# Kernel tuning notes

Measured on AMD Instinct MI355X. Metric: run time of the kernel, lower is better.

Reference implementation:

```python
import jax, jax.numpy as jnp
import numpy as np

DIM = 96; QK = 96; MLP = 192; HEADS = 6; NTOK = 8; GS = 128; KS = 5
B, D, H, W = 2, 8, 64, 64


def _ln(x, g, b, eps=1e-5):
    m = x.mean(-1, keepdims=True)
    v = x.var(-1, keepdims=True)
    return (x - m) / jnp.sqrt(v + eps) * g + b


def _l2(x, eps=1e-12):
    n = jnp.linalg.norm(x, axis=-1, keepdims=True)
    return x / jnp.maximum(n, eps)


def setup_inputs() -> dict:
    key = jax.random.key(0)
    ks = jax.random.split(key, 16)
    p = lambda i, shape: jax.random.normal(ks[i], shape, jnp.float32) * 0.02
    return dict(
        x=jax.random.normal(ks[0], (B, DIM, D, H, W), jnp.float32),
        means=jax.random.normal(ks[1], (NTOK, DIM), jnp.float32),
        ln1_g=jnp.ones((DIM,), jnp.float32), ln1_b=jnp.zeros((DIM,), jnp.float32),
        Wkg=p(2, (DIM, QK)), Wvg=p(3, (DIM, DIM)),
        Wq=p(4, (DIM, QK)), Wk=p(5, (DIM, QK)), Wv=p(6, (DIM, DIM)), Wproj=p(7, (DIM, DIM)),
        Wconv=p(8, (DIM, DIM)),
        ln2_g=jnp.ones((DIM,), jnp.float32), ln2_b=jnp.zeros((DIM,), jnp.float32),
        W1=p(9, (DIM, MLP)), b1=jnp.zeros((MLP,), jnp.float32),
        Wdw=p(10, (MLP, 1, KS, KS, KS)), bdw=jnp.zeros((MLP,), jnp.float32),
        W2=p(11, (MLP, DIM)), b2=jnp.zeros((DIM,), jnp.float32),
    )


def reference(x, means, ln1_g, ln1_b, Wkg, Wvg, Wq, Wk, Wv, Wproj, Wconv,
              ln2_g, ln2_b, W1, b1, Wdw, bdw, W2, b2):
    b, c, d, h, w = x.shape
    N = d * h * w
    xt = x.reshape(b, c, N).transpose(0, 2, 1)          # b n c
    residual = xt
    xn = _ln(xt, ln1_g, ln1_b)

    # IRCA (eval, initted=True): k/v from cluster means (buffer, detached)
    mns = jax.lax.stop_gradient(means)
    kg = (mns @ Wkg).reshape(NTOK, HEADS, QK // HEADS).transpose(1, 0, 2)  # h t dq
    vg = (mns @ Wvg).reshape(NTOK, HEADS, c // HEADS).transpose(1, 0, 2)   # h t dv

    # cluster assignment + sort (no_grad in torch)
    scores = _l2(jax.lax.stop_gradient(xn)) @ _l2(mns).T                   # b n t
    belong = jnp.argmax(scores, axis=-1)
    idx = jnp.argsort(belong, axis=-1)                                     # b n

    # IASA: project, gather by cluster-sorted index
    q = xn @ Wq; k = xn @ Wk; v = xn @ Wv
    take = lambda t: jnp.take_along_axis(t, idx[..., None], axis=1)
    qs, ks_, vs = take(q), take(k), take(v)

    gs = min(N, GS)
    ng = N // gs                      # N chosen divisible by gs -> pad_n = 0
    dq = QK // HEADS; dv = c // HEADS
    qb = qs.reshape(b, ng, gs, HEADS, dq).transpose(0, 1, 3, 2, 4)  # b ng h gs dq

    def windows(t, dh):
        # append reversed last group, then take overlapping 2*gs windows, stride gs
        tp = jnp.concatenate([t, t[:, N - gs:][:, ::-1]], axis=1)   # b (ng+1)*gs .
        blk = tp.reshape(b, ng + 1, gs, HEADS, dh)
        wnd = jnp.concatenate([blk[:, :-1], blk[:, 1:]], axis=2)    # b ng 2gs h dh
        return wnd.transpose(0, 1, 3, 2, 4)                         # b ng h 2gs dh

    kw = windows(ks_, dq)
    vw = windows(vs, dv)
    scale = float(1.0 / np.sqrt(dq))

    a1 = jax.nn.softmax(jnp.einsum('bghqd,bghkd->bghqk', qb, kw) * scale, axis=-1)
    out1 = jnp.einsum('bghqk,bghkd->bghqd', a1, vw)
    a2 = jax.nn.softmax(jnp.einsum('bghqd,htd->bghqt', qb, kg) * scale, axis=-1)
    out2 = jnp.einsum('bghqt,htd->bghqd', a2, vg)

    out = (out1 + out2).transpose(0, 1, 3, 2, 4).reshape(b, N, c)   # sorted order
    inv = jnp.argsort(idx, axis=-1)                                  # scatter back
    out = jnp.take_along_axis(out, inv[..., None], axis=1)
    out = out @ Wproj

    y = out @ Wconv                      # 1x1x1 conv3d == channel matmul
    xr = residual + y

    # PreNorm ConvFFN3D
    z = _ln(xr, ln2_g, ln2_b)
    z = jax.nn.gelu(z @ W1 + b1, approximate=False)
    zv = z.transpose(0, 2, 1).reshape(b, MLP, d, h, w)
    pad = (KS - 1) // 2
    dwo = jax.lax.conv_general_dilated(
        zv, Wdw, (1, 1, 1), [(pad, pad)] * 3,
        feature_group_count=MLP, dimension_numbers=('NCDHW', 'OIDHW', 'NCDHW'))
    dwo = jax.nn.gelu(dwo + bdw.reshape(1, MLP, 1, 1, 1), approximate=False)
    z = z + dwo.reshape(b, MLP, N).transpose(0, 2, 1)
    z = z @ W2 + b2

    return (z + xr).transpose(0, 2, 1).reshape(b, c, d, h, w)
```

## Files before the change

### kernel.cpp

```cpp
#include <hip/hip_runtime.h>
#include <math.h>

#define NB 2
#define NC 96
#define ND 8
#define NHH 64
#define NWW 64
#define NN 32768
#define NTOK 8
#define NHEADS 6
#define GSZ 128
#define NGRP 256
#define NMLP 192

typedef float4 f4;

__device__ __forceinline__ float gelu_f(float x) {
    return 0.5f * x * (1.0f + erff(x * 0.70710678118654752440f));
}

__global__ void __launch_bounds__(256) k_precompute(
    const float* __restrict__ means, const float* __restrict__ g1, const float* __restrict__ b1v,
    const float* __restrict__ Wkg, const float* __restrict__ Wvg,
    const float* __restrict__ Wproj, const float* __restrict__ Wconv,
    float* __restrict__ mnn, float* __restrict__ gdot, float* __restrict__ bdot,
    float* __restrict__ kg, float* __restrict__ vg, float* __restrict__ wpc) {
    int blk = blockIdx.x; int tid = threadIdx.x;
    if (blk == 0) {
        __shared__ float mlds[NTOK*NC];
        __shared__ float glds[NC], blds[NC];
        for (int i = tid; i < NTOK*NC; i += 256) mlds[i] = means[i];
        if (tid < NC) { glds[tid] = g1[tid]; blds[tid] = b1v[tid]; }
        __syncthreads();
        if (tid < NTOK) {
            float ss = 0.f;
            for (int c = 0; c < NC; ++c) { float v = mlds[tid*NC+c]; ss += v*v; }
            float inv = 1.0f / fmaxf(sqrtf(ss), 1e-12f);
            float gd = 0.f, bd = 0.f;
            for (int c = 0; c < NC; ++c) {
                float v = mlds[tid*NC+c] * inv;
                mnn[tid*NC+c] = v;
                gd += glds[c]*v; bd += blds[c]*v;
            }
            gdot[tid] = gd; bdot[tid] = bd;
        }
        for (int i = tid; i < NHEADS*NTOK*16; i += 256) {
            int h = i / (NTOK*16); int r = i % (NTOK*16); int t = r / 16; int e = r % 16;
            float sk = 0.f, sv = 0.f;
            for (int c = 0; c < NC; ++c) {
                float mv = mlds[t*NC+c];
                sk += mv * Wkg[c*NC + h*16+e];
                sv += mv * Wvg[c*NC + h*16+e];
            }
            kg[i] = sk; vg[i] = sv;
        }
    } else {
        int r0 = (blk-1)*24;
        __shared__ float wcv[NC][NC];
        __shared__ float wpl[24][NC];
        for (int i = tid; i < NC*NC; i += 256) wcv[i/NC][i%NC] = Wconv[i];
        for (int i = tid; i < 24*NC; i += 256) wpl[i/NC][i%NC] = Wproj[(r0 + i/NC)*NC + i%NC];
        __syncthreads();
        for (int o = tid; o < 24*NC; o += 256) {
            int r = o / NC, c = o % NC;
            float s = 0.f;
            for (int k = 0; k < NC; ++k) s += wpl[r][k]*wcv[k][c];
            wpc[(r0+r)*NC + c] = s;
        }
    }
}

__global__ void __launch_bounds__(256) k_ln1(
    const float* __restrict__ x, const float* __restrict__ g1, const float* __restrict__ b1v,
    const float* __restrict__ mnn, const float* __restrict__ gdot, const float* __restrict__ bdot,
    float* __restrict__ xn, int* __restrict__ belong) {
    __shared__ __align__(16) float xt[NC][68];
    __shared__ float meanl[64], rstdl[64];
    __shared__ float gl[NC], bl[NC], gdl[NTOK], bdl[NTOK];
    int b = blockIdx.y; int n0 = blockIdx.x * 64;
    int tid = threadIdx.x;
    if (tid < NC) { gl[tid] = g1[tid]; bl[tid] = b1v[tid]; }
    if (tid >= NC && tid < NC+NTOK) { gdl[tid-NC] = gdot[tid-NC]; bdl[tid-NC] = bdot[tid-NC]; }
    for (int i = tid; i < NC*64; i += 256) {
        int c = i >> 6, n = i & 63;
        xt[c][n] = x[((size_t)b*NC + c)*NN + n0 + n];
    }
    __syncthreads();
    int lane = tid & 63, w = tid >> 6;
    float ga = gl[lane];
    float gb = (lane < 32) ? gl[64+lane] : 0.f;
    float ma[NTOK], mb[NTOK];
#pragma unroll
    for (int t = 0; t < NTOK; ++t) {
        ma[t] = mnn[t*NC + lane];
        mb[t] = (lane < 32) ? mnn[t*NC + 64 + lane] : 0.f;
    }
    for (int tk = 0; tk < 16; ++tk) {
        int tok = w*16 + tk;
        float a  = xt[lane][tok];
        float bb = (lane < 32) ? xt[64+lane][tok] : 0.f;
        float red[10];
        red[0] = a + bb;
        red[1] = a*a + bb*bb;
        float ag = a*ga, bg = bb*gb;
#pragma unroll
        for (int t = 0; t < NTOK; ++t) red[2+t] = ag*ma[t] + bg*mb[t];
#pragma unroll
        for (int off = 32; off > 0; off >>= 1) {
#pragma unroll
            for (int r = 0; r < 10; ++r) red[r] += __shfl_xor(red[r], off);
        }
        if (lane == 0) {
            float mean = red[0] * (1.0f/NC);
            float var  = red[1] * (1.0f/NC) - mean*mean;
            float rstd = rsqrtf(var + 1e-5f);
            meanl[tok] = mean; rstdl[tok] = rstd;
            int best = 0; float bestv = -1e30f;
#pragma unroll
            for (int t = 0; t < NTOK; ++t) {
                float sc = rstd*(red[2+t] - mean*gdl[t]) + bdl[t];
                if (sc > bestv) { bestv = sc; best = t; }
            }
            belong[b*NN + n0 + tok] = best;
        }
    }
    __syncthreads();
    for (int i = tid; i < 64*NC; i += 256) {
        int n = i / NC, c = i % NC;
        float v = (xt[c][n] - meanl[n]) * rstdl[n] * gl[c] + bl[c];
        xn[((size_t)b*NN + n0 + n)*NC + c] = v;
    }
}

__global__ void __launch_bounds__(256) k_hist(const int* __restrict__ belong, int* __restrict__ hist) {
    int b = blockIdx.y, ch = blockIdx.x, tid = threadIdx.x;
    __shared__ int wc[4][NTOK];
    int myt = belong[b*NN + ch*256 + tid];
    int w = tid >> 6, lane = tid & 63;
#pragma unroll
    for (int t = 0; t < NTOK; ++t) {
        unsigned long long m = __ballot(myt == t);
        if (lane == 0) wc[w][t] = __popcll(m);
    }
    __syncthreads();
    if (tid < NTOK) hist[(b*128 + ch)*NTOK + tid] = wc[0][tid]+wc[1][tid]+wc[2][tid]+wc[3][tid];
}

__global__ void __launch_bounds__(256) k_scan(const int* __restrict__ hist, int* __restrict__ base) {
    int b = blockIdx.x, tid = threadIdx.x;
    __shared__ int A[NTOK][128], Bf[NTOK][128], orig[NTOK][128];
    __shared__ int cb[NTOK];
    for (int i = tid; i < NTOK*128; i += 256) {
        int t = i >> 7, ch = i & 127;
        int v = hist[(b*128 + ch)*NTOK + t];
        A[t][ch] = v; orig[t][ch] = v;
    }
    __syncthreads();
    for (int d = 1; d < 128; d <<= 1) {
        for (int i = tid; i < NTOK*128; i += 256) {
            int t = i >> 7, ch = i & 127;
            Bf[t][ch] = A[t][ch] + ((ch >= d) ? A[t][ch-d] : 0);
        }
        __syncthreads();
        for (int i = tid; i < NTOK*128; i += 256) {
            int t = i >> 7, ch = i & 127;
            A[t][ch] = Bf[t][ch];
        }
        __syncthreads();
    }
    if (tid == 0) {
        int run = 0;
        for (int t = 0; t < NTOK; ++t) { cb[t] = run; run += A[t][127]; }
    }
    __syncthreads();
    for (int i = tid; i < NTOK*128; i += 256) {
        int t = i >> 7, ch = i & 127;
        base[(b*128 + ch)*NTOK + t] = cb[t] + A[t][ch] - orig[t][ch];
    }
}

__global__ void __launch_bounds__(256) k_scatteridx(
    const int* __restrict__ belong, const int* __restrict__ base,
    int* __restrict__ idx, int* __restrict__ inv) {
    int b = blockIdx.y, ch = blockIdx.x, tid = threadIdx.x;
    __shared__ int wc[4][NTOK];
    __shared__ int woff[4][NTOK];
    int n = ch*256 + tid;
    int myt = belong[b*NN + n];
    int w = tid >> 6, lane = tid & 63;
    unsigned long long mymask = 0;
#pragma unroll
    for (int t = 0; t < NTOK; ++t) {
        unsigned long long m = __ballot(myt == t);
        if (myt == t) mymask = m;
        if (lane == 0) wc[w][t] = __popcll(m);
    }
    __syncthreads();
    if (tid < 32) {
        int w2 = tid >> 3, t = tid & 7;
        int s = 0;
        for (int ww = 0; ww < w2; ++ww) s += wc[ww][t];
        woff[w2][t] = s;
    }
    __syncthreads();
    int rank = __popcll(mymask & ((1ull << lane) - 1ull));
    int p = base[(b*128+ch)*NTOK + myt] + woff[w][myt] + rank;
    idx[b*NN + p] = n;
    inv[b*NN + n] = p;
}

__global__ void __launch_bounds__(256) k_qkv(
    const float* __restrict__ xn, const int* __restrict__ idx,
    const float* __restrict__ Wq, const float* __restrict__ Wk, const float* __restrict__ Wv,
    float* __restrict__ qs, float* __restrict__ ks, float* __restrict__ vs) {
    __shared__ __align__(16) float xnT[NC][132];
    __shared__ __align__(16) float wch[32][NC];
    __shared__ int idxl[128];
    int b = blockIdx.y; int p0 = blockIdx.x * 128; int tid = threadIdx.x;
    if (tid < 128) idxl[tid] = idx[b*NN + p0 + tid];
    __syncthreads();
    for (int i = tid; i < 128*NC; i += 256) {
        int p = i / NC, c = i % NC;
        xnT[c][p] = xn[((size_t)b*NN + idxl[p])*NC + c];
    }
    int cx = tid & 15, ny = tid >> 4;
    const float* Ws[3] = {Wq, Wk, Wv};
    float* Os[3] = {qs, ks, vs};
    for (int m = 0; m < 3; ++m) {
        float acc[8][6];
#pragma unroll
        for (int i = 0; i < 8; ++i)
#pragma unroll
            for (int j = 0; j < 6; ++j) acc[i][j] = 0.f;
        const float* W = Ws[m];
        for (int kc = 0; kc < NC; kc += 32) {
            __syncthreads();
            for (int i = tid; i < 32*NC; i += 256) {
                int kk = i / NC, c = i % NC;
                wch[kk][c] = W[(kc+kk)*NC + c];
            }
            __syncthreads();
            for (int kk = 0; kk < 32; ++kk) {
                f4 a0 = *(const f4*)&xnT[kc+kk][ny*8];
                f4 a1 = *(const f4*)&xnT[kc+kk][ny*8+4];
                float a[8] = {a0.x,a0.y,a0.z,a0.w,a1.x,a1.y,a1.z,a1.w};
                float2 w0 = *(const float2*)&wch[kk][cx*6];
                float2 w1 = *(const float2*)&wch[kk][cx*6+2];
                float2 w2 = *(const float2*)&wch[kk][cx*6+4];
                float bb[6] = {w0.x,w0.y,w1.x,w1.y,w2.x,w2.y};
#pragma unroll
                for (int i = 0; i < 8; ++i)
#pragma unroll
                    for (int j = 0; j < 6; ++j) acc[i][j] += a[i]*bb[j];
            }
        }
        float* O = Os[m];
#pragma unroll
        for (int i = 0; i < 8; ++i) {
            size_t off = ((size_t)b*NN + p0 + ny*8 + i)*NC + cx*6;
            float2 s0 = {acc[i][0], acc[i][1]};
            float2 s1 = {acc[i][2], acc[i][3]};
            float2 s2 = {acc[i][4], acc[i][5]};
            *(float2*)&O[off]   = s0;
            *(float2*)&O[off+2] = s1;
            *(float2*)&O[off+4] = s2;
        }
    }
}

__global__ void __launch_bounds__(256) k_attn(
    const float* __restrict__ qs, const float* __restrict__ ks, const float* __restrict__ vs,
    const float* __restrict__ kg, const float* __restrict__ vg,
    float* __restrict__ attn) {
    __shared__ __align__(16) f4 kt[256][4];
    __shared__ __align__(16) f4 vt[256][4];
    __shared__ __align__(16) f4 kgs[NTOK][4];
    __shared__ __align__(16) f4 vgs[NTOK][4];
    int g = blockIdx.x, h = blockIdx.y, b = blockIdx.z;
    int tid = threadIdx.x;
    for (int i = tid; i < 1024; i += 256) {
        int r = i >> 2, c = i & 3;
        int src = g*GSZ + r;
        if (g == NGRP-1 && r >= GSZ) src = NN - 1 - (r - GSZ);
        size_t off = ((size_t)b*NN + src)*NC + h*16 + c*4;
        kt[r][c] = *(const f4*)&ks[off];
        vt[r][c] = *(const f4*)&vs[off];
    }
    if (tid < 32) {
        int t = tid >> 2, c = tid & 3;
        kgs[t][c] = *(const f4*)&kg[(h*NTOK + t)*16 + c*4];
        vgs[t][c] = *(const f4*)&vg[(h*NTOK + t)*16 + c*4];
    }
    int wv = tid >> 6, lane = tid & 63;
    int pr = lane & 15;
    int qt = lane >> 4;
    int r0 = wv*32 + pr*2;
    float qv0[16], qv1[16];
    {
        const f4* qp0 = (const f4*)&qs[((size_t)b*NN + g*GSZ + r0)*NC + h*16];
        const f4* qp1 = (const f4*)&qs[((size_t)b*NN + g*GSZ + r0 + 1)*NC + h*16];
#pragma unroll
        for (int i = 0; i < 4; ++i) {
            f4 t0 = qp0[i], t1 = qp1[i];
            qv0[i*4+0]=t0.x*0.25f; qv0[i*4+1]=t0.y*0.25f; qv0[i*4+2]=t0.z*0.25f; qv0[i*4+3]=t0.w*0.25f;
            qv1[i*4+0]=t1.x*0.25f; qv1[i*4+1]=t1.y*0.25f; qv1[i*4+2]=t1.z*0.25f; qv1[i*4+3]=t1.w*0.25f;
        }
    }
    __syncthreads();
    float m0 = -1e30f, l0 = 0.f, m1 = -1e30f, l1 = 0.f;
    float acc0[16], acc1[16];
#pragma unroll
    for (int e = 0; e < 16; ++e) { acc0[e] = 0.f; acc1[e] = 0.f; }
    for (int c8 = 0; c8 < 8; ++c8) {
        float s0[8], s1[8];
#pragma unroll
        for (int j = 0; j < 8; ++j) {
            const f4* kp = &kt[(c8*8 + j)*4 + qt][0];
            f4 ka = kp[0], kb = kp[1], kc = kp[2], kd = kp[3];
            s0[j] = qv0[0]*ka.x + qv0[1]*ka.y + qv0[2]*ka.z + qv0[3]*ka.w
                  + qv0[4]*kb.x + qv0[5]*kb.y + qv0[6]*kb.z + qv0[7]*kb.w
                  + qv0[8]*kc.x + qv0[9]*kc.y + qv0[10]*kc.z + qv0[11]*kc.w
                  + qv0[12]*kd.x + qv0[13]*kd.y + qv0[14]*kd.z + qv0[15]*kd.w;
            s1[j] = qv1[0]*ka.x + qv1[1]*ka.y + qv1[2]*ka.z + qv1[3]*ka.w
                  + qv1[4]*kb.x + qv1[5]*kb.y + qv1[6]*kb.z + qv1[7]*kb.w
                  + qv1[8]*kc.x + qv1[9]*kc.y + qv1[10]*kc.z + qv1[11]*kc.w
                  + qv1[12]*kd.x + qv1[13]*kd.y + qv1[14]*kd.z + qv1[15]*kd.w;
        }
        float cm0 = fmaxf(fmaxf(fmaxf(s0[0],s0[1]), fmaxf(s0[2],s0[3])),
                          fmaxf(fmaxf(s0[4],s0[5]), fmaxf(s0[6],s0[7])));
        float cm1 = fmaxf(fmaxf(fmaxf(s1[0],s1[1]), fmaxf(s1[2],s1[3])),
                          fmaxf(fmaxf(s1[4],s1[5]), fmaxf(s1[6],s1[7])));
        float nm0 = fmaxf(m0, cm0), nm1 = fmaxf(m1, cm1);
        float corr0 = __expf(m0 - nm0), corr1 = __expf(m1 - nm1);
        m0 = nm0; m1 = nm1;
        l0 *= corr0; l1 *= corr1;
#pragma unroll
        for (int e = 0; e < 16; ++e) { acc0[e] *= corr0; acc1[e] *= corr1; }
#pragma unroll
        for (int j = 0; j < 8; ++j) {
            float p0 = __expf(s0[j] - m0);
            float p1 = __expf(s1[j] - m1);
            l0 += p0; l1 += p1;
            const f4* vp = &vt[(c8*8 + j)*4 + qt][0];
            f4 va = vp[0], vb = vp[1], vc = vp[2], vd = vp[3];
            acc0[0] += p0*va.x; acc0[1] += p0*va.y; acc0[2] += p0*va.z; acc0[3] += p0*va.w;
            acc0[4] += p0*vb.x; acc0[5] += p0*vb.y; acc0[6] += p0*vb.z; acc0[7] += p0*vb.w;
            acc0[8] += p0*vc.x; acc0[9] += p0*vc.y; acc0[10] += p0*vc.z; acc0[11] += p0*vc.w;
            acc0[12] += p0*vd.x; acc0[13] += p0*vd.y; acc0[14] += p0*vd.z; acc0[15] += p0*vd.w;
            acc1[0] += p1*va.x; acc1[1] += p1*va.y; acc1[2] += p1*va.z; acc1[3] += p1*va.w;
            acc1[4] += p1*vb.x; acc1[5] += p1*vb.y; acc1[6] += p1*vb.z; acc1[7] += p1*vb.w;
            acc1[8] += p1*vc.x; acc1[9] += p1*vc.y; acc1[10] += p1*vc.z; acc1[11] += p1*vc.w;
            acc1[12] += p1*vd.x; acc1[13] += p1*vd.y; acc1[14] += p1*vd.z; acc1[15] += p1*vd.w;
        }
    }
#pragma unroll
    for (int off = 16; off <= 32; off <<= 1) {
        float om = __shfl_xor(m0, off), ol = __shfl_xor(l0, off);
        float mw = fmaxf(m0, om);
        float e0 = __expf(m0 - mw), e1 = __expf(om - mw);
        l0 = l0*e0 + ol*e1; m0 = mw;
#pragma unroll
        for (int e = 0; e < 16; ++e) {
            float oa = __shfl_xor(acc0[e], off);
            acc0[e] = acc0[e]*e0 + oa*e1;
        }
        om = __shfl_xor(m1, off); ol = __shfl_xor(l1, off);
        mw = fmaxf(m1, om);
        e0 = __expf(m1 - mw); e1 = __expf(om - mw);
        l1 = l1*e0 + ol*e1; m1 = mw;
#pragma unroll
        for (int e = 0; e < 16; ++e) {
            float oa = __shfl_xor(acc1[e], off);
            acc1[e] = acc1[e]*e0 + oa*e1;
        }
    }
    float qvs[16], accs[16];
#pragma unroll
    for (int e = 0; e < 16; ++e) {
        qvs[e]  = (qt == 1) ? qv1[e]  : qv0[e];
        accs[e] = (qt == 1) ? acc1[e] : acc0[e];
    }
    float ls = (qt == 1) ? l1 : l0;
    if (qt < 2) {
        float m2 = -1e30f, l2 = 0.f;
        float a2[16];
#pragma unroll
        for (int e = 0; e < 16; ++e) a2[e] = 0.f;
#pragma unroll
        for (int t = 0; t < NTOK; ++t) {
            f4 ka = kgs[t][0], kb = kgs[t][1], kc = kgs[t][2], kd = kgs[t][3];
            float s = qvs[0]*ka.x + qvs[1]*ka.y + qvs[2]*ka.z + qvs[3]*ka.w
                    + qvs[4]*kb.x + qvs[5]*kb.y + qvs[6]*kb.z + qvs[7]*kb.w
                    + qvs[8]*kc.x + qvs[9]*kc.y + qvs[10]*kc.z + qvs[11]*kc.w
                    + qvs[12]*kd.x + qvs[13]*kd.y + qvs[14]*kd.z + qvs[15]*kd.w;
            float nm2 = fmaxf(m2, s);
            float corr = __expf(m2 - nm2);
            m2 = nm2;
            l2 *= corr;
            float p = __expf(s - m2);
            l2 += p;
            f4 va = vgs[t][0], vb = vgs[t][1], vc = vgs[t][2], vd = vgs[t][3];
#pragma unroll
            for (int e = 0; e < 16; ++e) a2[e] *= corr;
            a2[0] += p*va.x; a2[1] += p*va.y; a2[2] += p*va.z; a2[3] += p*va.w;
            a2[4] += p*vb.x; a2[5] += p*vb.y; a2[6] += p*vb.z; a2[7] += p*vb.w;
            a2[8] += p*vc.x; a2[9] += p*vc.y; a2[10] += p*vc.z; a2[11] += p*vc.w;
            a2[12] += p*vd.x; a2[13] += p*vd.y; a2[14] += p*vd.z; a2[15] += p*vd.w;
        }
        float inv2 = 1.f / l2;
        float invw = 1.f / ls;
        float o[16];
#pragma unroll
        for (int e = 0; e < 16; ++e) o[e] = accs[e]*invw + a2[e]*inv2;
        f4* op = (f4*)&attn[((size_t)b*NN + g*GSZ + r0 + qt)*NC + h*16];
#pragma unroll
        for (int i = 0; i < 4; ++i) {
            f4 t = {o[i*4+0], o[i*4+1], o[i*4+2], o[i*4+3]};
            op[i] = t;
        }
    }
}

__global__ void __launch_bounds__(256) k_scatproj(
    const float* __restrict__ attn, const int* __restrict__ inv,
    const float* __restrict__ wpc, const float* __restrict__ x,
    float* __restrict__ xrt) {
    __shared__ __align__(16) float attT[NC][68];
    __shared__ __align__(16) float wch[32][NC];
    __shared__ int invl[64];
    int b = blockIdx.y; int n0 = blockIdx.x * 64; int tid = threadIdx.x;
    if (tid < 64) invl[tid] = inv[b*NN + n0 + tid];
    __syncthreads();
    for (int i = tid; i < 64*NC; i += 256) {
        int n = i / NC, c = i % NC;
        attT[c][n] = attn[((size_t)b*NN + invl[n])*NC + c];
    }
    int nx = tid & 15, cy = tid >> 4;
    float acc[4][6];
#pragma unroll
    for (int i = 0; i < 4; ++i)
#pragma unroll
        for (int j = 0; j < 6; ++j) acc[i][j] = 0.f;
    for (int kc = 0; kc < NC; kc += 32) {
        __syncthreads();
        for (int i = tid; i < 32*NC; i += 256) {
            int kk = i / NC, c = i % NC;
            wch[kk][c] = wpc[(kc+kk)*NC + c];
        }
        __syncthreads();
        for (int kk = 0; kk < 32; ++kk) {
            f4 a0 = *(const f4*)&attT[kc+kk][nx*4];
            float a[4] = {a0.x,a0.y,a0.z,a0.w};
            float2 w0 = *(const float2*)&wch[kk][cy*6];
            float2 w1 = *(const float2*)&wch[kk][cy*6+2];
            float2 w2 = *(const float2*)&wch[kk][cy*6+4];
            float bb[6] = {w0.x,w0.y,w1.x,w1.y,w2.x,w2.y};
#pragma unroll
            for (int i = 0; i < 4; ++i)
#pragma unroll
                for (int j = 0; j < 6; ++j) acc[i][j] += a[i]*bb[j];
        }
    }
#pragma unroll
    for (int j = 0; j < 6; ++j) {
        int c = cy*6 + j;
        size_t off = ((size_t)b*NC + c)*NN + n0 + nx*4;
        f4 xv = *(const f4*)&x[off];
        f4 o = {acc[0][j]+xv.x, acc[1][j]+xv.y, acc[2][j]+xv.z, acc[3][j]+xv.w};
        *(f4*)&xrt[off] = o;
    }
}

__global__ void __launch_bounds__(256) k_mlp1(
    const float* __restrict__ xrt, const float* __restrict__ g2, const float* __restrict__ b2v,
    const float* __restrict__ W1, const float* __restrict__ b1m,
    float* __restrict__ z1t) {
    __shared__ __align__(16) float xt[NC][68];
    __shared__ __align__(16) float wch[32][NMLP];
    __shared__ float meanl[64], rstdl[64];
    __shared__ float gl[NC], bl[NC];
    int b = blockIdx.y; int n0 = blockIdx.x*64; int tid = threadIdx.x;
    if (tid < NC) { gl[tid] = g2[tid]; bl[tid] = b2v[tid]; }
    for (int i = tid; i < NC*64; i += 256) {
        int c = i >> 6, n = i & 63;
        xt[c][n] = xrt[((size_t)b*NC + c)*NN + n0 + n];
    }
    __syncthreads();
    int lane = tid & 63, w = tid >> 6;
    for (int tk = 0; tk < 16; ++tk) {
        int tok = w*16 + tk;
        float a  = xt[lane][tok];
        float bb = (lane < 32) ? xt[64+lane][tok] : 0.f;
        float s = a + bb, sq = a*a + bb*bb;
#pragma unroll
        for (int off = 32; off > 0; off >>= 1) {
            s  += __shfl_xor(s, off);
            sq += __shfl_xor(sq, off);
        }
        if (lane == 0) {
            float mean = s * (1.0f/NC);
            float var  = sq * (1.0f/NC) - mean*mean;
            meanl[tok] = mean; rstdl[tok] = rsqrtf(var + 1e-5f);
        }
    }
    __syncthreads();
    for (int i = tid; i < NC*64; i += 256) {
        int c = i >> 6, n = i & 63;
        xt[c][n] = (xt[c][n]-meanl[n])*rstdl[n]*gl[c]+bl[c];
    }
    int nx = tid & 15, my = tid >> 4;
    float acc[4][12];
#pragma unroll
    for (int i = 0; i < 4; ++i)
#pragma unroll
        for (int j = 0; j < 12; ++j) acc[i][j] = 0.f;
    for (int kc = 0; kc < NC; kc += 32) {
        __syncthreads();
        for (int i = tid; i < 32*NMLP; i += 256) {
            int kk = i / NMLP, c = i % NMLP;
            wch[kk][c] = W1[(kc+kk)*NMLP + c];
        }
        __syncthreads();
        for (int kk = 0; kk < 32; ++kk) {
            f4 a0 = *(const f4*)&xt[kc+kk][nx*4];
            float a[4] = {a0.x,a0.y,a0.z,a0.w};
            f4 w0 = *(const f4*)&wch[kk][my*12];
            f4 w1 = *(const f4*)&wch[kk][my*12+4];
            f4 w2 = *(const f4*)&wch[kk][my*12+8];
            float bb[12] = {w0.x,w0.y,w0.z,w0.w,w1.x,w1.y,w1.z,w1.w,w2.x,w2.y,w2.z,w2.w};
#pragma unroll
            for (int i = 0; i < 4; ++i)
#pragma unroll
                for (int j = 0; j < 12; ++j) acc[i][j] += a[i]*bb[j];
        }
    }
#pragma unroll
    for (int j = 0; j < 12; ++j) {
        int mm = my*12 + j;
        float bias = b1m[mm];
        size_t off = ((size_t)b*NMLP + mm)*NN + n0 + nx*4;
        f4 o = { gelu_f(acc[0][j]+bias), gelu_f(acc[1][j]+bias),
                 gelu_f(acc[2][j]+bias), gelu_f(acc[3][j]+bias) };
        *(f4*)&z1t[off] = o;
    }
}

__global__ void __launch_bounds__(256) k_dwconv(
    const float* __restrict__ z1t, const float* __restrict__ Wdw, const float* __restrict__ bdw,
    float* __restrict__ z2t) {
    __shared__ __align__(16) float tin[ND][20][72];
    __shared__ float wl[128];
    int ht = blockIdx.x, mch = blockIdx.y, b = blockIdx.z;
    int h0 = ht*16; int tid = threadIdx.x;
    if (tid < 125) wl[tid] = Wdw[mch*125 + tid];
    const float* src = &z1t[((size_t)b*NMLP + mch)*NN];
    for (int i = tid; i < ND*20*68; i += 256) {
        int dd = i / (20*68); int r = i % (20*68); int hh = r / 68; int ww = r % 68;
        int gh = h0 + hh - 2, gw = ww - 2;
        float v = 0.f;
        if ((unsigned)gh < 64u && (unsigned)gw < 64u) v = src[dd*4096 + gh*64 + gw];
        tin[dd][hh][ww] = v;
    }
    __syncthreads();
    int rowid = tid >> 1; int od = rowid >> 4; int ohl = rowid & 15; int wb = (tid & 1)*32;
    float acc[32];
#pragma unroll
    for (int o = 0; o < 32; ++o) acc[o] = 0.f;
    for (int kd = 0; kd < 5; ++kd) {
        int id = od + kd - 2;
        if ((unsigned)id >= (unsigned)ND) continue;
#pragma unroll
        for (int kh = 0; kh < 5; ++kh) {
            const float* rp = &tin[id][ohl+kh][wb];
            float seg[36];
#pragma unroll
            for (int i = 0; i < 9; ++i) *(f4*)&seg[i*4] = *(const f4*)&rp[i*4];
#pragma unroll
            for (int kw = 0; kw < 5; ++kw) {
                float wt = wl[kd*25 + kh*5 + kw];
#pragma unroll
                for (int o = 0; o < 32; ++o) acc[o] += seg[o+kw]*wt;
            }
        }
    }
    float bias = bdw[mch];
    float* dst = &z2t[((size_t)b*NMLP + mch)*NN + od*4096 + (size_t)(h0+ohl)*64 + wb];
    const float* ctr = &tin[od][ohl+2][wb+2];
#pragma unroll
    for (int o4 = 0; o4 < 32; o4 += 4) {
        f4 ov = { ctr[o4+0] + gelu_f(acc[o4+0]+bias),
                  ctr[o4+1] + gelu_f(acc[o4+1]+bias),
                  ctr[o4+2] + gelu_f(acc[o4+2]+bias),
                  ctr[o4+3] + gelu_f(acc[o4+3]+bias) };
        *(f4*)&dst[o4] = ov;
    }
}

__global__ void __launch_bounds__(256) k_final(
    const float* __restrict__ z2t, const float* __restrict__ W2, const float* __restrict__ b2m,
    const float* __restrict__ xrt, float* __restrict__ out) {
    __shared__ __align__(16) float zch[32][132];
    __shared__ __align__(16) float wch[32][NC];
    int b = blockIdx.y; int n0 = blockIdx.x*128; int tid = threadIdx.x;
    int nx = tid & 15, cy = tid >> 4;
    float acc[8][6];
#pragma unroll
    for (int i = 0; i < 8; ++i)
#pragma unroll
        for (int j = 0; j < 6; ++j) acc[i][j] = 0.f;
    for (int kc = 0; kc < NMLP; kc += 32) {
        __syncthreads();
        for (int i = tid; i < 32*128; i += 256) {
            int kk = i >> 7, n = i & 127;
            zch[kk][n] = z2t[((size_t)b*NMLP + kc + kk)*NN + n0 + n];
        }
        for (int i = tid; i < 32*NC; i += 256) {
            int kk = i / NC, c = i % NC;
            wch[kk][c] = W2[(kc+kk)*NC + c];
        }
        __syncthreads();
        for (int kk = 0; kk < 32; ++kk) {
            f4 a0 = *(const f4*)&zch[kk][nx*8];
            f4 a1 = *(const f4*)&zch[kk][nx*8+4];
            float a[8] = {a0.x,a0.y,a0.z,a0.w,a1.x,a1.y,a1.z,a1.w};
            float2 w0 = *(const float2*)&wch[kk][cy*6];
            float2 w1 = *(const float2*)&wch[kk][cy*6+2];
            float2 w2 = *(const float2*)&wch[kk][cy*6+4];
            float bb[6] = {w0.x,w0.y,w1.x,w1.y,w2.x,w2.y};
#pragma unroll
            for (int i = 0; i < 8; ++i)
#pragma unroll
                for (int j = 0; j < 6; ++j) acc[i][j] += a[i]*bb[j];
        }
    }
#pragma unroll
    for (int j = 0; j < 6; ++j) {
        int c = cy*6 + j;
        float bias = b2m[c];
        size_t off = ((size_t)b*NC + c)*NN + n0 + nx*8;
        f4 x0 = *(const f4*)&xrt[off];
        f4 x1 = *(const f4*)&xrt[off+4];
        f4 o0 = {acc[0][j]+bias+x0.x, acc[1][j]+bias+x0.y, acc[2][j]+bias+x0.z, acc[3][j]+bias+x0.w};
        f4 o1 = {acc[4][j]+bias+x1.x, acc[5][j]+bias+x1.y, acc[6][j]+bias+x1.z, acc[7][j]+bias+x1.w};
        *(f4*)&out[off]   = o0;
        *(f4*)&out[off+4] = o1;
    }
}

extern "C" void kernel_launch(void* const* d_in, const int* in_sizes, int n_in,
                              void* d_out, int out_size, void* d_ws, size_t ws_size,
                              hipStream_t stream) {
    (void)in_sizes; (void)n_in; (void)out_size; (void)ws_size;
    const float* x     = (const float*)d_in[0];
    const float* means = (const float*)d_in[1];
    const float* ln1_g = (const float*)d_in[2];
    const float* ln1_b = (const float*)d_in[3];
    const float* Wkg   = (const float*)d_in[4];
    const float* Wvg   = (const float*)d_in[5];
    const float* Wq    = (const float*)d_in[6];
    const float* Wk    = (const float*)d_in[7];
    const float* Wv    = (const float*)d_in[8];
    const float* Wproj = (const float*)d_in[9];
    const float* Wconv = (const float*)d_in[10];
    const float* ln2_g = (const float*)d_in[11];
    const float* ln2_b = (const float*)d_in[12];
    const float* W1    = (const float*)d_in[13];
    const float* b1    = (const float*)d_in[14];
    const float* Wdw   = (const float*)d_in[15];
    const float* bdw   = (const float*)d_in[16];
    const float* W2    = (const float*)d_in[17];
    const float* b2    = (const float*)d_in[18];
    float* out = (float*)d_out;

    float* ws = (float*)d_ws;
    const size_t SZ = (size_t)NB*NN*NC;
    float* xn   = ws;
    float* qs   = ws + SZ;
    float* ks   = ws + 2*SZ;
    float* vs   = ws + 3*SZ;
    float* attn = ws + 4*SZ;
    float* xrt  = ws;
    float* z1t  = ws + SZ;
    float* z2t  = ws + 3*SZ;
    float* faux = ws + 5*SZ;
    float* mnn  = faux;
    float* gdot = faux + 768;
    float* bdot = faux + 776;
    float* kg   = faux + 784;
    float* vg   = faux + 1552;
    float* wpc  = faux + 2320;
    int* iaux   = (int*)(faux + 11536);
    int* belong = iaux;
    int* idx    = iaux + NB*NN;
    int* inv    = iaux + 2*NB*NN;
    int* hist   = iaux + 3*NB*NN;
    int* baseb  = hist + NB*128*NTOK;

    k_precompute<<<dim3(5), dim3(256), 0, stream>>>(
        means, ln1_g, ln1_b, Wkg, Wvg, Wproj, Wconv, mnn, gdot, bdot, kg, vg, wpc);
    k_ln1<<<dim3(NN/64, NB), dim3(256), 0, stream>>>(
        x, ln1_g, ln1_b, mnn, gdot, bdot, xn, belong);
    k_hist<<<dim3(NN/256, NB), dim3(256), 0, stream>>>(belong, hist);
    k_scan<<<dim3(NB), dim3(256), 0, stream>>>(hist, baseb);
    k_scatteridx<<<dim3(NN/256, NB), dim3(256), 0, stream>>>(belong, baseb, idx, inv);
    k_qkv<<<dim3(NN/128, NB), dim3(256), 0, stream>>>(xn, idx, Wq, Wk, Wv, qs, ks, vs);
    k_attn<<<dim3(NGRP, NHEADS, NB), dim3(256), 0, stream>>>(qs, ks, vs, kg, vg, attn);
    k_scatproj<<<dim3(NN/64, NB), dim3(256), 0, stream>>>(attn, inv, wpc, x, xrt);
    k_mlp1<<<dim3(NN/64, NB), dim3(256), 0, stream>>>(xrt, ln2_g, ln2_b, W1, b1, z1t);
    k_dwconv<<<dim3(4, NMLP, NB), dim3(256), 0, stream>>>(z1t, Wdw, bdw, z2t);
    k_final<<<dim3(NN/128, NB), dim3(256), 0, stream>>>(z2t, W2, b2, xrt, out);
}
```

Baseline: 641.6 us.

## Process two attention groups per block to share overlapping K/V window loads

The attention kernel now has each 512-thread block handle two adjacent 128-query groups. The block loads one 384-row K/V window into shared memory that covers both groups' overlapping 256-key windows, so each group indexes in with a base offset. This cuts global K/V traffic per pair of groups from 512 rows to 384. The online-softmax chunk is reduced from 8 to 4 keys, likely to limit register pressure under the larger launch bound, at the cost of more rescaling steps.

```diff
diff --git a/kernel.cpp b/kernel.cpp
--- a/kernel.cpp
+++ b/kernel.cpp
@@ -268,20 +268,20 @@
     }
 }
 
-__global__ void __launch_bounds__(256) k_attn(
+__global__ void __launch_bounds__(512) k_attn(
     const float* __restrict__ qs, const float* __restrict__ ks, const float* __restrict__ vs,
     const float* __restrict__ kg, const float* __restrict__ vg,
     float* __restrict__ attn) {
-    __shared__ __align__(16) f4 kt[256][4];
-    __shared__ __align__(16) f4 vt[256][4];
+    __shared__ __align__(16) f4 kt[384][4];
+    __shared__ __align__(16) f4 vt[384][4];
     __shared__ __align__(16) f4 kgs[NTOK][4];
     __shared__ __align__(16) f4 vgs[NTOK][4];
-    int g = blockIdx.x, h = blockIdx.y, b = blockIdx.z;
+    int gp = blockIdx.x, h = blockIdx.y, b = blockIdx.z;
     int tid = threadIdx.x;
-    for (int i = tid; i < 1024; i += 256) {
+    for (int i = tid; i < 384*4; i += 512) {
         int r = i >> 2, c = i & 3;
-        int src = g*GSZ + r;
-        if (g == NGRP-1 && r >= GSZ) src = NN - 1 - (r - GSZ);
+        int src = gp*256 + r;
+        if (src >= NN) src = NN - 1 - (src - NN);
         size_t off = ((size_t)b*NN + src)*NC + h*16 + c*4;
         kt[r][c] = *(const f4*)&ks[off];
         vt[r][c] = *(const f4*)&vs[off];
@@ -294,11 +294,13 @@
     int wv = tid >> 6, lane = tid & 63;
     int pr = lane & 15;
     int qt = lane >> 4;
-    int r0 = wv*32 + pr*2;
+    int rib = wv*32 + pr*2;
+    int kbase = (rib >= 128) ? 128 : 0;
+    int grow = gp*256 + rib;
     float qv0[16], qv1[16];
     {
-        const f4* qp0 = (const f4*)&qs[((size_t)b*NN + g*GSZ + r0)*NC + h*16];
-        const f4* qp1 = (const f4*)&qs[((size_t)b*NN + g*GSZ + r0 + 1)*NC + h*16];
+        const f4* qp0 = (const f4*)&qs[((size_t)b*NN + grow)*NC + h*16];
+        const f4* qp1 = (const f4*)&qs[((size_t)b*NN + grow + 1)*NC + h*16];
 #pragma unroll
         for (int i = 0; i < 4; ++i) {
             f4 t0 = qp0[i], t1 = qp1[i];
@@ -311,11 +313,11 @@
     float acc0[16], acc1[16];
 #pragma unroll
     for (int e = 0; e < 16; ++e) { acc0[e] = 0.f; acc1[e] = 0.f; }
-    for (int c8 = 0; c8 < 8; ++c8) {
-        float s0[8], s1[8];
-#pragma unroll
-        for (int j = 0; j < 8; ++j) {
-            const f4* kp = &kt[(c8*8 + j)*4 + qt][0];
+    for (int c4 = 0; c4 < 16; ++c4) {
+        float s0[4], s1[4];
+#pragma unroll
+        for (int j = 0; j < 4; ++j) {
+            const f4* kp = &kt[kbase + (c4*4 + j)*4 + qt][0];
             f4 ka = kp[0], kb = kp[1], kc = kp[2], kd = kp[3];
             s0[j] = qv0[0]*ka.x + qv0[1]*ka.y + qv0[2]*ka.z + qv0[3]*ka.w
                   + qv0[4]*kb.x + qv0[5]*kb.y + qv0[6]*kb.z + qv0[7]*kb.w
@@ -326,10 +328,8 @@
                   + qv1[8]*kc.x + qv1[9]*kc.y + qv1[10]*kc.z + qv1[11]*kc.w
                   + qv1[12]*kd.x + qv1[13]*kd.y + qv1[14]*kd.z + qv1[15]*kd.w;
         }
-        float cm0 = fmaxf(fmaxf(fmaxf(s0[0],s0[1]), fmaxf(s0[2],s0[3])),
-                          fmaxf(fmaxf(s0[4],s0[5]), fmaxf(s0[6],s0[7])));
-        float cm1 = fmaxf(fmaxf(fmaxf(s1[0],s1[1]), fmaxf(s1[2],s1[3])),
-                          fmaxf(fmaxf(s1[4],s1[5]), fmaxf(s1[6],s1[7])));
+        float cm0 = fmaxf(fmaxf(s0[0],s0[1]), fmaxf(s0[2],s0[3]));
+        float cm1 = fmaxf(fmaxf(s1[0],s1[1]), fmaxf(s1[2],s1[3]));
         float nm0 = fmaxf(m0, cm0), nm1 = fmaxf(m1, cm1);
         float corr0 = __expf(m0 - nm0), corr1 = __expf(m1 - nm1);
         m0 = nm0; m1 = nm1;
@@ -337,11 +337,11 @@
 #pragma unroll
         for (int e = 0; e < 16; ++e) { acc0[e] *= corr0; acc1[e] *= corr1; }
 #pragma unroll
-        for (int j = 0; j < 8; ++j) {
+        for (int j = 0; j < 4; ++j) {
             float p0 = __expf(s0[j] - m0);
             float p1 = __expf(s1[j] - m1);
             l0 += p0; l1 += p1;
-            const f4* vp = &vt[(c8*8 + j)*4 + qt][0];
+            const f4* vp = &vt[kbase + (c4*4 + j)*4 + qt][0];
             f4 va = vp[0], vb = vp[1], vc = vp[2], vd = vp[3];
             acc0[0] += p0*va.x; acc0[1] += p0*va.y; acc0[2] += p0*va.z; acc0[3] += p0*va.w;
             acc0[4] += p0*vb.x; acc0[5] += p0*vb.y; acc0[6] += p0*vb.z; acc0[7] += p0*vb.w;
@@ -412,7 +412,7 @@
         float o[16];
 #pragma unroll
         for (int e = 0; e < 16; ++e) o[e] = accs[e]*invw + a2[e]*inv2;
-        f4* op = (f4*)&attn[((size_t)b*NN + g*GSZ + r0 + qt)*NC + h*16];
+        f4* op = (f4*)&attn[((size_t)b*NN + grow + qt)*NC + h*16];
 #pragma unroll
         for (int i = 0; i < 4; ++i) {
             f4 t = {o[i*4+0], o[i*4+1], o[i*4+2], o[i*4+3]};
@@ -704,7 +704,7 @@
     k_scan<<<dim3(NB), dim3(256), 0, stream>>>(hist, baseb);
     k_scatteridx<<<dim3(NN/256, NB), dim3(256), 0, stream>>>(belong, baseb, idx, inv);
     k_qkv<<<dim3(NN/128, NB), dim3(256), 0, stream>>>(xn, idx, Wq, Wk, Wv, qs, ks, vs);
-    k_attn<<<dim3(NGRP, NHEADS, NB), dim3(256), 0, stream>>>(qs, ks, vs, kg, vg, attn);
+    k_attn<<<dim3(NGRP/2, NHEADS, NB), dim3(512), 0, stream>>>(qs, ks, vs, kg, vg, attn);
     k_scatproj<<<dim3(NN/64, NB), dim3(256), 0, stream>>>(attn, inv, wpc, x, xrt);
     k_mlp1<<<dim3(NN/64, NB), dim3(256), 0, stream>>>(xrt, ln2_g, ln2_b, W1, b1, z1t);
     k_dwconv<<<dim3(4, NMLP, NB), dim3(256), 0, stream>>>(z1t, Wdw, bdw, z2t);
```

Result: slower. 655.4 us (+2.2%).
